# Kernel optimization log

Measured on AMD Instinct MI355X. Metric: run time of the kernel, lower is better.

## Reference

```python
import jax, jax.numpy as jnp
import numpy as np

# 5x5 Sobel kernels (exact constants from the torch module)
_GX5 = np.array([[2.,1.,1e-6,-1.,-2.],[3.,2.,1e-6,-2.,-3.],[4.,3.,0.,-3.,-4.],[3.,2.,1e-6,-2.,-3.],[2.,1.,1e-6,-1.,-2.]], np.float32)
_GY5 = np.array([[2.,3.,4.,3.,2.],[1.,2.,3.,2.,1.],[1e-6,1e-6,1e-6,1e-6,1e-6],[-1.,-2.,-3.,-2.,-1.],[-2.,-3.,-4.,-3.,-2.]], np.float32)


def _sobel(x):  # x: [B,1,H,W] -> [B,2,H,W] (gx, gy)
    k = jnp.stack([jnp.asarray(_GX5), jnp.asarray(_GY5)])[:, None]  # [2,1,5,5]
    return jax.lax.conv_general_dilated(x, k, (1, 1), 'SAME',
                                        dimension_numbers=('NCHW', 'OIHW', 'NCHW'))


def _quantize(gx, gy):
    # OrientQuantize: magnitude + orientation quantized to 8 bins
    div = 3.1416 / 8.0
    mag = jnp.sqrt(gx * gx + gy * gy + 1e-8)
    o = jnp.arctan2(gy, gx)
    conds = [
        (o >= div) & (o < 3 * div),
        (o >= 3 * div) & (o < 5 * div),
        (o >= 5 * div) & (o < 7 * div),
        ((o >= 7 * div) & (o < 8 * div)) | ((o >= -8 * div) & (o < -7 * div)),
        (o >= -7 * div) & (o < -5 * div),
        (o >= -5 * div) & (o < -3 * div),
        (o >= -3 * div) & (o < -div),
        (o >= -div) & (o < div),
    ]
    q = jnp.select(conds, [jnp.full_like(o, float(i)) for i in range(8)], 3.0)
    return mag, q.astype(jnp.int32)


def setup_inputs() -> dict:
    key = jax.random.key(0)
    k1, k2, k3 = jax.random.split(key, 3)
    return {
        'seg_map': jax.random.normal(k1, (2, 21, 256, 256), jnp.float32),
        'dense_ft': jax.random.normal(k2, (2, 256, 256, 256), jnp.float32),
        'mask': jax.random.normal(k3, (2, 21, 256, 256), jnp.float32),
        'label_with_bg': jnp.ones((2, 21), jnp.float32),
    }


def reference(seg_map, dense_ft, mask, label_with_bg):
    BETA, K, STEP = 1000.0, 100, 5
    n, C, h, w = seg_map.shape
    nfg, ch, hw = C - 1, dense_ft.shape[1], h * w

    # ---- Mix_fg: per-class Sobel orientation edges on sharpened softmax ----
    seg = jax.nn.softmax(seg_map * BETA, axis=1)[:, 1:]            # [n,nfg,h,w]
    edges = _sobel(seg.reshape(n * nfg, 1, h, w)).reshape(n, nfg, 2, h, w)
    label_fg = label_with_bg[:, 1:]                                 # [n,nfg]
    edges = edges * label_fg[:, :, None, None, None]
    mag, q = _quantize(edges[:, :, 0], edges[:, :, 1])              # [n,nfg,h,w]

    # ---- boundary pixels: strongest-K edge magnitudes per (b,c) ----
    _, pos = jax.lax.top_k(mag.reshape(n, nfg, hw), K)              # [n,nfg,K]
    o = jnp.take_along_axis(q.reshape(n, nfg, hw), pos, -1) + 1     # 1..8

    # ---- in_out_div: walk STEP pixels along/against gradient orientation ----
    mod4 = ((o % 4) == 0).astype(jnp.int32)
    horiz = ((o == 2) | (o == 6)).astype(jnp.int32)
    p_out = jnp.where(o < 4, STEP * STEP, -STEP)   # (-STEP)**(1+(o<4))
    p_in = jnp.where(o < 4, -STEP, 1)              # (-STEP)**(o<4)
    s_out = jnp.where(o % 2 == 0, -1, 1)           # (-1)**(1+o)
    s_in = -s_out                                   # (-1)**o
    out_idx = pos + p_out * mod4 * w + s_out * horiz
    in_idx = pos + p_in * mod4 * w + s_in * horiz

    def valid(x):
        return (x % (w - 1) != 0) & (x % (w - 1) != 1) & (x > 0) & (x < hw - 1)

    v_out, v_in = valid(out_idx), valid(in_idx)                     # [n,nfg,K] bool
    oi = jnp.clip(out_idx, 0, hw - 1)
    ii = jnp.clip(in_idx, 0, hw - 1)

    # ---- gather features / mask probs at walked positions ----
    dense = jax.nn.softmax(dense_ft, axis=1).reshape(n, ch, hw)
    msk = jax.nn.softmax(mask, axis=1).reshape(n, C, hw)
    b = jnp.arange(n)[:, None, None]
    outs = dense[b, :, oi]                                          # [n,nfg,K,ch]
    ins = jax.lax.stop_gradient(dense[b, :, ii])                    # detached
    outs_m = jax.lax.stop_gradient(msk[b, :, oi])
    ins_m = jax.lax.stop_gradient(msk[b, :, ii])

    sim = jnp.einsum('bcie,bcje->bcij', outs, ins)                  # [n,nfg,K,K]
    sim_m = jnp.einsum('bcie,bcje->bcij', outs_m, ins_m)

    fvi = v_in.astype(sim.dtype)
    fvo = v_out.astype(sim.dtype)
    ci = jnp.maximum(fvi.sum(-1), 1.0)
    co = jnp.maximum(fvo.sum(-1), 1.0)

    def rowmean(s):  # mean over in-samples -> [n,nfg,K]
        return (s * fvi[:, :, None, :]).sum(-1) / ci[..., None]

    def colmean(s):  # mean over out-samples -> [n,nfg,K]
        return (s * fvo[:, :, :, None]).sum(-2) / co[..., None]

    def gmean(s):    # global masked mean -> [n,nfg]
        num = (s * fvo[:, :, :, None] * fvi[:, :, None, :]).sum((-2, -1))
        return num / jnp.maximum(fvo.sum(-1) * fvi.sum(-1), 1.0)

    def beacon(sgn_mask, sgn_dense, vals, v):
        # loss_constructor: signed masked means over FP/FN/TP/TN categories
        def term(cat, sign):
            m = (cat & v).astype(vals.dtype)
            cnt = m.sum(-1)
            return sign * jnp.where(cnt > 0, (vals * m).sum(-1) / jnp.maximum(cnt, 1.0), 0.0)
        FP = sgn_mask & ~sgn_dense
        FN = ~sgn_mask & sgn_dense
        TP = ~sgn_mask & ~sgn_dense
        TN = sgn_mask & sgn_dense
        return term(FP, -1.0) + term(FN, 1.0) + term(TP, 1.0) + term(TN, -1.0)

    g = gmean(sim)
    gm = gmean(sim_m)
    rm, rmm = rowmean(sim), rowmean(sim_m)
    cm, cmm = colmean(sim), colmean(sim_m)
    sgn_rm = jax.lax.stop_gradient(rm) > g[..., None]
    sgn_rmm = rmm > gm[..., None]
    sgn_cm = jax.lax.stop_gradient(cm) > g[..., None]
    sgn_cmm = cmm > gm[..., None]

    loss_bc = beacon(sgn_rmm, sgn_rm, rm, v_out) + beacon(sgn_cmm, sgn_cm, cm, v_in)
    gate = ((v_in.sum(-1) >= 10) & (v_out.sum(-1) >= 10)).astype(loss_bc.dtype)
    gate = gate * (label_fg > 0).astype(loss_bc.dtype)
    return (loss_bc * gate).sum()
```

## Files before the change

kernel.cpp:

```cpp
#include <hip/hip_runtime.h>
#include <math.h>

#define HW 65536
#define WID 256
#define HEI 256
#define NB 2
#define NFG 20
#define NMAP 40
#define CH 256
#define CSEG 21
#define TK 100
#define PARTS 32
#define PARTN (HW / PARTS)
#define RPP (HEI / PARTS)
#define CAND (PARTS * TK)

__device__ __constant__ float c_GX[25] = {
  2.f,1.f,1e-6f,-1.f,-2.f,
  3.f,2.f,1e-6f,-2.f,-3.f,
  4.f,3.f,0.f,-3.f,-4.f,
  3.f,2.f,1e-6f,-2.f,-3.f,
  2.f,1.f,1e-6f,-1.f,-2.f};
__device__ __constant__ float c_GY[25] = {
  2.f,3.f,4.f,3.f,2.f,
  1.f,2.f,3.f,2.f,1.f,
  1e-6f,1e-6f,1e-6f,1e-6f,1e-6f,
  -1.f,-2.f,-3.f,-2.f,-1.f,
  -2.f,-3.f,-4.f,-3.f,-2.f};

__global__ __launch_bounds__(256) void k_seg(const float* __restrict__ seg_map,
                                             double* __restrict__ seg) {
  int idx = blockIdx.x * blockDim.x + threadIdx.x;
  if (idx >= NB * HW) return;
  int b = idx / HW, p = idx % HW;
  double x[CSEG];
  double m = -INFINITY;
  #pragma unroll
  for (int c = 0; c < CSEG; ++c) {
    double v = (double)seg_map[(size_t)(b * CSEG + c) * HW + p] * 1000.0;
    x[c] = v;
    m = fmax(m, v);
  }
  double s = 0.0;
  #pragma unroll
  for (int c = 0; c < CSEG; ++c) { double e = exp(x[c] - m); x[c] = e; s += e; }
  #pragma unroll
  for (int c = 1; c < CSEG; ++c)
    seg[(size_t)(b * NFG + (c - 1)) * HW + p] = x[c] / s;
}

__global__ __launch_bounds__(256) void k_sobel_topk(
    const double* __restrict__ seg, const float* __restrict__ label,
    unsigned char* __restrict__ qb,
    unsigned long long* __restrict__ ckey, int* __restrict__ cidx) {
  int mapi = blockIdx.x / PARTS, part = blockIdx.x % PARTS;
  int tid = threadIdx.x;
  int lane = tid & 63, w = tid >> 6;
  int row0 = part * RPP;
  const double* im = seg + (size_t)mapi * HW;

  __shared__ double tile[RPP + 4][WID];
  __shared__ unsigned int hist4[4][256];
  __shared__ int sfx[256];
  __shared__ int wtot[4];
  __shared__ int s_r, s_cnt, s_bsel;

  for (int r = 0; r < RPP + 4; ++r) {
    int gr = row0 - 2 + r;
    tile[r][tid] = (gr >= 0 && gr < HEI) ? im[gr * WID + tid] : 0.0;
  }
  if (tid == 0) { s_r = TK; s_cnt = 0; }
  __syncthreads();

  int b = mapi / NFG, c = mapi % NFG;
  double lab = (double)label[b * CSEG + c + 1];
  const double DIVQ = 3.1416 / 8.0;
  const double T1 = DIVQ, T3 = 3.0*DIVQ, T5 = 5.0*DIVQ, T7 = 7.0*DIVQ, T8 = 8.0*DIVQ;

  unsigned long long mykey[RPP];
  #pragma unroll
  for (int k = 0; k < RPP; ++k) {
    double gx = 0.0, gy = 0.0;
    #pragma unroll
    for (int dy = 0; dy < 5; ++dy) {
      #pragma unroll
      for (int dx = 0; dx < 5; ++dx) {
        int xx = tid + dx - 2;
        double v = (xx >= 0 && xx < WID) ? tile[k + dy][xx] : 0.0;
        gx += v * (double)c_GX[dy * 5 + dx];
        gy += v * (double)c_GY[dy * 5 + dx];
      }
    }
    gx *= lab; gy *= lab;
    double mg = sqrt(gx * gx + gy * gy + 1e-8);
    double o = atan2(gy, gx);
    int qv;
    if (o >= T1 && o < T3) qv = 0;
    else if (o >= T3 && o < T5) qv = 1;
    else if (o >= T5 && o < T7) qv = 2;
    else if ((o >= T7 && o < T8) || (o >= -T8 && o < -T7)) qv = 3;
    else if (o >= -T7 && o < -T5) qv = 4;
    else if (o >= -T5 && o < -T3) qv = 5;
    else if (o >= -T3 && o < -T1) qv = 6;
    else if (o >= -T1 && o < T1) qv = 7;
    else qv = 3;
    mykey[k] = (unsigned long long)__double_as_longlong(mg);
    qb[(size_t)mapi * HW + (size_t)(row0 + k) * WID + tid] = (unsigned char)qv;
  }
  __syncthreads();
  unsigned long long* sk = (unsigned long long*)&tile[0][0];
  #pragma unroll
  for (int k = 0; k < RPP; ++k) sk[k * WID + tid] = mykey[k];
  __syncthreads();

  unsigned long long pfx = 0ull, msk = 0ull;
  for (int round = 0; round < 8; ++round) {
    int shift = 56 - 8 * round;
    hist4[0][tid] = 0; hist4[1][tid] = 0; hist4[2][tid] = 0; hist4[3][tid] = 0;
    __syncthreads();
    #pragma unroll
    for (int k = 0; k < RPP; ++k) {
      unsigned long long key = sk[k * WID + tid];
      if ((key & msk) == pfx)
        atomicAdd(&hist4[w][(unsigned int)(key >> shift) & 0xFFu], 1u);
    }
    __syncthreads();
    int r = s_r;
    int v = (int)(hist4[0][tid] + hist4[1][tid] + hist4[2][tid] + hist4[3][tid]);
    #pragma unroll
    for (int off = 1; off < 64; off <<= 1) {
      int u = __shfl_down(v, off, 64);
      if (lane + off < 64) v += u;
    }
    if (lane == 0) wtot[w] = v;
    __syncthreads();
    int add = 0;
    for (int ww = w + 1; ww < 4; ++ww) add += wtot[ww];
    v += add;
    sfx[tid] = v;
    __syncthreads();
    int above = (tid == 255) ? 0 : sfx[tid + 1];
    if (v >= r && above < r) { s_bsel = tid; s_r = r - above; }
    __syncthreads();
    pfx |= ((unsigned long long)s_bsel << shift);
    msk |= (0xFFull << shift);
  }
  unsigned long long kv = pfx;
  int need_eq = s_r;

  unsigned long long* outk = ckey + (size_t)mapi * CAND + (size_t)part * TK;
  int* outi = cidx + (size_t)mapi * CAND + (size_t)part * TK;
  int gbase = part * PARTN;
  const int CHN = PARTN / 256;
  int base = tid * CHN;
  int myeq = 0;
  for (int k = 0; k < CHN; ++k) {
    unsigned long long key = sk[base + k];
    if (key > kv) {
      int slot = atomicAdd(&s_cnt, 1);
      outk[slot] = key; outi[slot] = gbase + base + k;
    } else if (key == kv) ++myeq;
  }
  int v2 = myeq;
  #pragma unroll
  for (int off = 1; off < 64; off <<= 1) {
    int u = __shfl_up(v2, off, 64);
    if (lane >= off) v2 += u;
  }
  if (lane == 63) wtot[w] = v2;
  __syncthreads();
  int addl = 0;
  for (int ww = 0; ww < w; ++ww) addl += wtot[ww];
  int incl = v2 + addl;
  int rank = incl - myeq;
  int eqtot = wtot[0] + wtot[1] + wtot[2] + wtot[3];
  int lo = eqtot - need_eq;
  int wb = TK - need_eq;
  for (int k = 0; k < CHN; ++k) {
    unsigned long long key = sk[base + k];
    if (key == kv) {
      if (rank >= lo) { outk[wb + rank - lo] = key; outi[wb + rank - lo] = gbase + base + k; }
      ++rank;
    }
  }
}

__global__ __launch_bounds__(256) void k_topk_merge(
    const unsigned long long* __restrict__ ckey,
    const int* __restrict__ cidx, int* __restrict__ pos) {
  int mapi = blockIdx.x, tid = threadIdx.x;
  int lane = tid & 63, w = tid >> 6;
  __shared__ unsigned long long k_[CAND];
  __shared__ int i_[CAND];
  __shared__ int eqi[CAND];
  __shared__ unsigned int hist4[4][256];
  __shared__ int sfx[256];
  __shared__ int wtot[4];
  __shared__ int s_r, s_cnt, s_eqn, s_bsel;
  for (int c = tid; c < CAND; c += 256) {
    k_[c] = ckey[(size_t)mapi * CAND + c];
    i_[c] = cidx[(size_t)mapi * CAND + c];
  }
  if (tid == 0) { s_r = TK; s_cnt = 0; s_eqn = 0; }
  __syncthreads();
  unsigned long long pfx = 0ull, msk = 0ull;
  for (int round = 0; round < 8; ++round) {
    int shift = 56 - 8 * round;
    hist4[0][tid] = 0; hist4[1][tid] = 0; hist4[2][tid] = 0; hist4[3][tid] = 0;
    __syncthreads();
    for (int c = tid; c < CAND; c += 256) {
      unsigned long long key = k_[c];
      if ((key & msk) == pfx)
        atomicAdd(&hist4[w][(unsigned int)(key >> shift) & 0xFFu], 1u);
    }
    __syncthreads();
    int r = s_r;
    int v = (int)(hist4[0][tid] + hist4[1][tid] + hist4[2][tid] + hist4[3][tid]);
    #pragma unroll
    for (int off = 1; off < 64; off <<= 1) {
      int u = __shfl_down(v, off, 64);
      if (lane + off < 64) v += u;
    }
    if (lane == 0) wtot[w] = v;
    __syncthreads();
    int add = 0;
    for (int ww = w + 1; ww < 4; ++ww) add += wtot[ww];
    v += add;
    sfx[tid] = v;
    __syncthreads();
    int above = (tid == 255) ? 0 : sfx[tid + 1];
    if (v >= r && above < r) { s_bsel = tid; s_r = r - above; }
    __syncthreads();
    pfx |= ((unsigned long long)s_bsel << shift);
    msk |= (0xFFull << shift);
  }
  unsigned long long kv = pfx;
  int need_eq = s_r;
  for (int c = tid; c < CAND; c += 256) {
    unsigned long long key = k_[c];
    if (key > kv) {
      int slot = atomicAdd(&s_cnt, 1);
      pos[mapi * TK + slot] = i_[c];
    } else if (key == kv) {
      int e = atomicAdd(&s_eqn, 1);
      eqi[e] = i_[c];
    }
  }
  __syncthreads();
  int eqn = s_eqn;
  int wb = TK - need_eq;
  for (int e = tid; e < eqn; e += 256) {
    int myi = eqi[e];
    int bigger = 0;
    for (int f = 0; f < eqn; ++f) bigger += (eqi[f] > myi) ? 1 : 0;
    if (bigger < need_eq) pos[mapi * TK + wb + bigger] = myi;
  }
}

__global__ __launch_bounds__(256) void k_gather(
    const float* __restrict__ dense_ft, const float* __restrict__ maskp,
    const unsigned char* __restrict__ qb, const int* __restrict__ pos,
    double* __restrict__ outs, double* __restrict__ ins,
    double* __restrict__ outs_m, double* __restrict__ ins_m,
    int* __restrict__ voutArr, int* __restrict__ vinArr) {
  int blk = blockIdx.x;
  int mapi = blk / TK, j = blk % TK;
  int b = mapi / NFG;
  int tid = threadIdx.x;
  int p = pos[mapi * TK + j];
  int o = (int)qb[(size_t)mapi * HW + p] + 1;
  int mod4 = ((o & 3) == 0) ? 1 : 0;
  int horiz = (o == 2 || o == 6) ? 1 : 0;
  int po = (o < 4) ? 25 : -5;
  int pi = (o < 4) ? -5 : 1;
  int so = ((o & 1) == 0) ? -1 : 1;
  int si = -so;
  int out_idx = p + po * mod4 * WID + so * horiz;
  int in_idx  = p + pi * mod4 * WID + si * horiz;
  int ro = out_idx % 255; if (ro < 0) ro += 255;
  int ri = in_idx  % 255; if (ri < 0) ri += 255;
  int vo = (ro != 0 && ro != 1 && out_idx > 0 && out_idx < HW - 1) ? 1 : 0;
  int vi = (ri != 0 && ri != 1 && in_idx  > 0 && in_idx  < HW - 1) ? 1 : 0;
  int oi = out_idx < 0 ? 0 : (out_idx > HW - 1 ? HW - 1 : out_idx);
  int ii = in_idx  < 0 ? 0 : (in_idx  > HW - 1 ? HW - 1 : in_idx);
  if (tid == 0) { voutArr[mapi * TK + j] = vo; vinArr[mapi * TK + j] = vi; }

  __shared__ double red[256];
  {
    double x = (double)dense_ft[(size_t)(b * CH + tid) * HW + oi];
    red[tid] = x; __syncthreads();
    for (int s = 128; s > 0; s >>= 1) { if (tid < s) red[tid] = fmax(red[tid], red[tid + s]); __syncthreads(); }
    double mx = red[0]; __syncthreads();
    double e = exp(x - mx);
    red[tid] = e; __syncthreads();
    for (int s = 128; s > 0; s >>= 1) { if (tid < s) red[tid] += red[tid + s]; __syncthreads(); }
    double sm = red[0]; __syncthreads();
    outs[((size_t)mapi * TK + j) * CH + tid] = e / sm;
  }
  {
    double x = (double)dense_ft[(size_t)(b * CH + tid) * HW + ii];
    red[tid] = x; __syncthreads();
    for (int s = 128; s > 0; s >>= 1) { if (tid < s) red[tid] = fmax(red[tid], red[tid + s]); __syncthreads(); }
    double mx = red[0]; __syncthreads();
    double e = exp(x - mx);
    red[tid] = e; __syncthreads();
    for (int s = 128; s > 0; s >>= 1) { if (tid < s) red[tid] += red[tid + s]; __syncthreads(); }
    double sm = red[0]; __syncthreads();
    ins[((size_t)mapi * TK + j) * CH + tid] = e / sm;
  }
  {
    double y = (tid < CSEG) ? (double)maskp[(size_t)(b * CSEG + tid) * HW + oi] : -INFINITY;
    red[tid] = y; __syncthreads();
    for (int s = 128; s > 0; s >>= 1) { if (tid < s) red[tid] = fmax(red[tid], red[tid + s]); __syncthreads(); }
    double mx = red[0]; __syncthreads();
    double e = (tid < CSEG) ? exp(y - mx) : 0.0;
    red[tid] = e; __syncthreads();
    for (int s = 128; s > 0; s >>= 1) { if (tid < s) red[tid] += red[tid + s]; __syncthreads(); }
    double sm = red[0]; __syncthreads();
    if (tid < CSEG) outs_m[((size_t)mapi * TK + j) * CSEG + tid] = e / sm;
    __syncthreads();
  }
  {
    double y = (tid < CSEG) ? (double)maskp[(size_t)(b * CSEG + tid) * HW + ii] : -INFINITY;
    red[tid] = y; __syncthreads();
    for (int s = 128; s > 0; s >>= 1) { if (tid < s) red[tid] = fmax(red[tid], red[tid + s]); __syncthreads(); }
    double mx = red[0]; __syncthreads();
    double e = (tid < CSEG) ? exp(y - mx) : 0.0;
    red[tid] = e; __syncthreads();
    for (int s = 128; s > 0; s >>= 1) { if (tid < s) red[tid] += red[tid + s]; __syncthreads(); }
    double sm = red[0]; __syncthreads();
    if (tid < CSEG) ins_m[((size_t)mapi * TK + j) * CSEG + tid] = e / sm;
  }
}

__global__ __launch_bounds__(256) void k_stats(
    const double* __restrict__ outs, const double* __restrict__ ins,
    const double* __restrict__ outs_m, const double* __restrict__ ins_m,
    const int* __restrict__ voutArr, const int* __restrict__ vinArr,
    const float* __restrict__ label, double* __restrict__ lossmap) {
  int mapi = blockIdx.x, tid = threadIdx.x;
  int b = mapi / NFG, c = mapi % NFG;
  __shared__ double fvo[TK], fvi[TK];
  __shared__ double avi[CH], avo[CH], avim[CSEG], avom[CSEG];
  __shared__ double rm[TK], cm[TK], rmm[TK], cmm[TK];
  __shared__ double s_sfvo, s_sfvi;
  if (tid < TK) {
    fvo[tid] = (double)voutArr[mapi * TK + tid];
    fvi[tid] = (double)vinArr[mapi * TK + tid];
  }
  __syncthreads();
  if (tid == 0) {
    double a = 0.0, d = 0.0;
    for (int j2 = 0; j2 < TK; ++j2) { a += fvo[j2]; d += fvi[j2]; }
    s_sfvo = a; s_sfvi = d;
  }
  const double* OUT  = outs   + (size_t)mapi * TK * CH;
  const double* IN   = ins    + (size_t)mapi * TK * CH;
  const double* OUTm = outs_m + (size_t)mapi * TK * CSEG;
  const double* INm  = ins_m  + (size_t)mapi * TK * CSEG;
  {
    double a = 0.0, d = 0.0;
    for (int j2 = 0; j2 < TK; ++j2) {
      a += IN[j2 * CH + tid] * fvi[j2];
      d += OUT[j2 * CH + tid] * fvo[j2];
    }
    avi[tid] = a; avo[tid] = d;
  }
  if (tid < CSEG) {
    double a = 0.0, d = 0.0;
    for (int j2 = 0; j2 < TK; ++j2) {
      a += INm[j2 * CSEG + tid] * fvi[j2];
      d += OUTm[j2 * CSEG + tid] * fvo[j2];
    }
    avim[tid] = a; avom[tid] = d;
  }
  __syncthreads();
  double ci = fmax(s_sfvi, 1.0), co = fmax(s_sfvo, 1.0);
  if (tid < TK) {
    double d1 = 0.0, d2 = 0.0, d3 = 0.0, d4 = 0.0;
    for (int e = 0; e < CH; ++e) { d1 += OUT[tid * CH + e] * avi[e]; d2 += IN[tid * CH + e] * avo[e]; }
    for (int e = 0; e < CSEG; ++e) { d3 += OUTm[tid * CSEG + e] * avim[e]; d4 += INm[tid * CSEG + e] * avom[e]; }
    rm[tid] = d1 / ci; cm[tid] = d2 / co; rmm[tid] = d3 / ci; cmm[tid] = d4 / co;
  }
  __syncthreads();
  if (tid == 0) {
    double g = 0.0, gm = 0.0;
    for (int e = 0; e < CH; ++e) g += avo[e] * avi[e];
    for (int e = 0; e < CSEG; ++e) gm += avom[e] * avim[e];
    double den = fmax(s_sfvo * s_sfvi, 1.0);
    g /= den; gm /= den;
    double loss = 0.0;
    {
      double s[4] = {0, 0, 0, 0}, cn[4] = {0, 0, 0, 0};
      for (int j2 = 0; j2 < TK; ++j2) {
        int smv = rmm[j2] > gm;
        int dmv = rm[j2] > g;
        int cat = smv ? (dmv ? 3 : 0) : (dmv ? 1 : 2);
        s[cat] += rm[j2] * fvo[j2];
        cn[cat] += fvo[j2];
      }
      const double sg[4] = {-1.0, 1.0, 1.0, -1.0};
      for (int t = 0; t < 4; ++t)
        if (cn[t] > 0.0) loss += sg[t] * (s[t] / fmax(cn[t], 1.0));
    }
    {
      double s[4] = {0, 0, 0, 0}, cn[4] = {0, 0, 0, 0};
      for (int j2 = 0; j2 < TK; ++j2) {
        int smv = cmm[j2] > gm;
        int dmv = cm[j2] > g;
        int cat = smv ? (dmv ? 3 : 0) : (dmv ? 1 : 2);
        s[cat] += cm[j2] * fvi[j2];
        cn[cat] += fvi[j2];
      }
      const double sg[4] = {-1.0, 1.0, 1.0, -1.0};
      for (int t = 0; t < 4; ++t)
        if (cn[t] > 0.0) loss += sg[t] * (s[t] / fmax(cn[t], 1.0));
    }
    float lab = label[b * CSEG + c + 1];
    double gate = (s_sfvi >= 10.0 && s_sfvo >= 10.0 && lab > 0.f) ? 1.0 : 0.0;
    lossmap[mapi] = loss * gate;
  }
}

__global__ __launch_bounds__(64) void k_final(const double* __restrict__ lossmap,
                                              float* __restrict__ out) {
  if (threadIdx.x == 0 && blockIdx.x == 0) {
    double s = 0.0;
    for (int i = 0; i < NMAP; ++i) s += lossmap[i];
    out[0] = (float)s;
  }
}

extern "C" void kernel_launch(void* const* d_in, const int* in_sizes, int n_in,
                              void* d_out, int out_size, void* d_ws, size_t ws_size,
                              hipStream_t stream) {
  const float* seg_map  = (const float*)d_in[0];
  const float* dense_ft = (const float*)d_in[1];
  const float* maskp    = (const float*)d_in[2];
  const float* label    = (const float*)d_in[3];
  float* outp = (float*)d_out;

  char* w = (char*)d_ws;
  double* seg = (double*)w;               w += (size_t)NB * NFG * HW * 8;
  double* outs   = (double*)w;            w += (size_t)NMAP * TK * CH * 8;
  double* ins    = (double*)w;            w += (size_t)NMAP * TK * CH * 8;
  double* outs_m = (double*)w;            w += (size_t)NMAP * TK * CSEG * 8;
  double* ins_m  = (double*)w;            w += (size_t)NMAP * TK * CSEG * 8;
  double* lossmap = (double*)w;           w += (size_t)NMAP * 8;
  unsigned long long* ckey = (unsigned long long*)w; w += (size_t)NMAP * CAND * 8;
  int* cidx = (int*)w;                    w += (size_t)NMAP * CAND * 4;
  int* pos  = (int*)w;                    w += (size_t)NMAP * TK * 4;
  int* vout = (int*)w;                    w += (size_t)NMAP * TK * 4;
  int* vin  = (int*)w;                    w += (size_t)NMAP * TK * 4;
  unsigned char* qb = (unsigned char*)w;  w += (size_t)NMAP * HW;

  k_seg<<<(NB * HW + 255) / 256, 256, 0, stream>>>(seg_map, seg);
  k_sobel_topk<<<NMAP * PARTS, 256, 0, stream>>>(seg, label, qb, ckey, cidx);
  k_topk_merge<<<NMAP, 256, 0, stream>>>(ckey, cidx, pos);
  k_gather<<<NMAP * TK, 256, 0, stream>>>(dense_ft, maskp, qb, pos, outs, ins,
                                          outs_m, ins_m, vout, vin);
  k_stats<<<NMAP, 256, 0, stream>>>(outs, ins, outs_m, ins_m, vout, vin, label, lossmap);
  k_final<<<1, 64, 0, stream>>>(lossmap, outp);
}
```

Baseline: 215.6 us.

## Replace barrier-heavy softmax reductions with per-wavefront shuffles and trim radix-select syncs

The gather/softmax kernel previously ran four block-wide tree reductions, each with many __syncthreads. It now gives each of the four wavefronts one softmax and reduces with 64-lane xor shuffles, with no block barriers. The radix-select loops in both top-k kernels zero the histogram once up front and clear it after reading, which drops one barrier and the shared suffix array per round. The per-pixel top-k also reads keys from registers instead of LDS, and the segmentation softmax skips exp for strongly underflowing inputs. Each wavefront now loads 4 strided dense_ft values per lane.

```diff
diff --git a/kernel.cpp b/kernel.cpp
--- a/kernel.cpp
+++ b/kernel.cpp
@@ -43,7 +43,11 @@
   }
   double s = 0.0;
   #pragma unroll
-  for (int c = 0; c < CSEG; ++c) { double e = exp(x[c] - m); x[c] = e; s += e; }
+  for (int c = 0; c < CSEG; ++c) {
+    double d = x[c] - m;
+    double e = (d < -746.0) ? 0.0 : exp(d);
+    x[c] = e; s += e;
+  }
   #pragma unroll
   for (int c = 1; c < CSEG; ++c)
     seg[(size_t)(b * NFG + (c - 1)) * HW + p] = x[c] / s;
@@ -61,7 +65,6 @@
 
   __shared__ double tile[RPP + 4][WID];
   __shared__ unsigned int hist4[4][256];
-  __shared__ int sfx[256];
   __shared__ int wtot[4];
   __shared__ int s_r, s_cnt, s_bsel;
 
@@ -69,6 +72,7 @@
     int gr = row0 - 2 + r;
     tile[r][tid] = (gr >= 0 && gr < HEI) ? im[gr * WID + tid] : 0.0;
   }
+  hist4[0][tid] = 0; hist4[1][tid] = 0; hist4[2][tid] = 0; hist4[3][tid] = 0;
   if (tid == 0) { s_r = TK; s_cnt = 0; }
   __syncthreads();
 
@@ -116,17 +120,17 @@
   unsigned long long pfx = 0ull, msk = 0ull;
   for (int round = 0; round < 8; ++round) {
     int shift = 56 - 8 * round;
-    hist4[0][tid] = 0; hist4[1][tid] = 0; hist4[2][tid] = 0; hist4[3][tid] = 0;
-    __syncthreads();
     #pragma unroll
     for (int k = 0; k < RPP; ++k) {
-      unsigned long long key = sk[k * WID + tid];
+      unsigned long long key = mykey[k];
       if ((key & msk) == pfx)
         atomicAdd(&hist4[w][(unsigned int)(key >> shift) & 0xFFu], 1u);
     }
     __syncthreads();
     int r = s_r;
-    int v = (int)(hist4[0][tid] + hist4[1][tid] + hist4[2][tid] + hist4[3][tid]);
+    int cnt = (int)(hist4[0][tid] + hist4[1][tid] + hist4[2][tid] + hist4[3][tid]);
+    hist4[0][tid] = 0; hist4[1][tid] = 0; hist4[2][tid] = 0; hist4[3][tid] = 0;
+    int v = cnt;
     #pragma unroll
     for (int off = 1; off < 64; off <<= 1) {
       int u = __shfl_down(v, off, 64);
@@ -137,10 +141,7 @@
     int add = 0;
     for (int ww = w + 1; ww < 4; ++ww) add += wtot[ww];
     v += add;
-    sfx[tid] = v;
-    __syncthreads();
-    int above = (tid == 255) ? 0 : sfx[tid + 1];
-    if (v >= r && above < r) { s_bsel = tid; s_r = r - above; }
+    if (v >= r && v - cnt < r) { s_bsel = tid; s_r = r - (v - cnt); }
     __syncthreads();
     pfx |= ((unsigned long long)s_bsel << shift);
     msk |= (0xFFull << shift);
@@ -194,20 +195,18 @@
   __shared__ int i_[CAND];
   __shared__ int eqi[CAND];
   __shared__ unsigned int hist4[4][256];
-  __shared__ int sfx[256];
   __shared__ int wtot[4];
   __shared__ int s_r, s_cnt, s_eqn, s_bsel;
   for (int c = tid; c < CAND; c += 256) {
     k_[c] = ckey[(size_t)mapi * CAND + c];
     i_[c] = cidx[(size_t)mapi * CAND + c];
   }
+  hist4[0][tid] = 0; hist4[1][tid] = 0; hist4[2][tid] = 0; hist4[3][tid] = 0;
   if (tid == 0) { s_r = TK; s_cnt = 0; s_eqn = 0; }
   __syncthreads();
   unsigned long long pfx = 0ull, msk = 0ull;
   for (int round = 0; round < 8; ++round) {
     int shift = 56 - 8 * round;
-    hist4[0][tid] = 0; hist4[1][tid] = 0; hist4[2][tid] = 0; hist4[3][tid] = 0;
-    __syncthreads();
     for (int c = tid; c < CAND; c += 256) {
       unsigned long long key = k_[c];
       if ((key & msk) == pfx)
@@ -215,7 +214,9 @@
     }
     __syncthreads();
     int r = s_r;
-    int v = (int)(hist4[0][tid] + hist4[1][tid] + hist4[2][tid] + hist4[3][tid]);
+    int cnt = (int)(hist4[0][tid] + hist4[1][tid] + hist4[2][tid] + hist4[3][tid]);
+    hist4[0][tid] = 0; hist4[1][tid] = 0; hist4[2][tid] = 0; hist4[3][tid] = 0;
+    int v = cnt;
     #pragma unroll
     for (int off = 1; off < 64; off <<= 1) {
       int u = __shfl_down(v, off, 64);
@@ -226,10 +227,7 @@
     int add = 0;
     for (int ww = w + 1; ww < 4; ++ww) add += wtot[ww];
     v += add;
-    sfx[tid] = v;
-    __syncthreads();
-    int above = (tid == 255) ? 0 : sfx[tid + 1];
-    if (v >= r && above < r) { s_bsel = tid; s_r = r - above; }
+    if (v >= r && v - cnt < r) { s_bsel = tid; s_r = r - (v - cnt); }
     __syncthreads();
     pfx |= ((unsigned long long)s_bsel << shift);
     msk |= (0xFFull << shift);
@@ -267,6 +265,7 @@
   int mapi = blk / TK, j = blk % TK;
   int b = mapi / NFG;
   int tid = threadIdx.x;
+  int lane = tid & 63, w = tid >> 6;
   int p = pos[mapi * TK + j];
   int o = (int)qb[(size_t)mapi * HW + p] + 1;
   int mod4 = ((o & 3) == 0) ? 1 : 0;
@@ -285,51 +284,38 @@
   int ii = in_idx  < 0 ? 0 : (in_idx  > HW - 1 ? HW - 1 : in_idx);
   if (tid == 0) { voutArr[mapi * TK + j] = vo; vinArr[mapi * TK + j] = vi; }
 
-  __shared__ double red[256];
-  {
-    double x = (double)dense_ft[(size_t)(b * CH + tid) * HW + oi];
-    red[tid] = x; __syncthreads();
-    for (int s = 128; s > 0; s >>= 1) { if (tid < s) red[tid] = fmax(red[tid], red[tid + s]); __syncthreads(); }
-    double mx = red[0]; __syncthreads();
-    double e = exp(x - mx);
-    red[tid] = e; __syncthreads();
-    for (int s = 128; s > 0; s >>= 1) { if (tid < s) red[tid] += red[tid + s]; __syncthreads(); }
-    double sm = red[0]; __syncthreads();
-    outs[((size_t)mapi * TK + j) * CH + tid] = e / sm;
-  }
-  {
-    double x = (double)dense_ft[(size_t)(b * CH + tid) * HW + ii];
-    red[tid] = x; __syncthreads();
-    for (int s = 128; s > 0; s >>= 1) { if (tid < s) red[tid] = fmax(red[tid], red[tid + s]); __syncthreads(); }
-    double mx = red[0]; __syncthreads();
-    double e = exp(x - mx);
-    red[tid] = e; __syncthreads();
-    for (int s = 128; s > 0; s >>= 1) { if (tid < s) red[tid] += red[tid + s]; __syncthreads(); }
-    double sm = red[0]; __syncthreads();
-    ins[((size_t)mapi * TK + j) * CH + tid] = e / sm;
-  }
-  {
-    double y = (tid < CSEG) ? (double)maskp[(size_t)(b * CSEG + tid) * HW + oi] : -INFINITY;
-    red[tid] = y; __syncthreads();
-    for (int s = 128; s > 0; s >>= 1) { if (tid < s) red[tid] = fmax(red[tid], red[tid + s]); __syncthreads(); }
-    double mx = red[0]; __syncthreads();
-    double e = (tid < CSEG) ? exp(y - mx) : 0.0;
-    red[tid] = e; __syncthreads();
-    for (int s = 128; s > 0; s >>= 1) { if (tid < s) red[tid] += red[tid + s]; __syncthreads(); }
-    double sm = red[0]; __syncthreads();
-    if (tid < CSEG) outs_m[((size_t)mapi * TK + j) * CSEG + tid] = e / sm;
-    __syncthreads();
-  }
-  {
-    double y = (tid < CSEG) ? (double)maskp[(size_t)(b * CSEG + tid) * HW + ii] : -INFINITY;
-    red[tid] = y; __syncthreads();
-    for (int s = 128; s > 0; s >>= 1) { if (tid < s) red[tid] = fmax(red[tid], red[tid + s]); __syncthreads(); }
-    double mx = red[0]; __syncthreads();
-    double e = (tid < CSEG) ? exp(y - mx) : 0.0;
-    red[tid] = e; __syncthreads();
-    for (int s = 128; s > 0; s >>= 1) { if (tid < s) red[tid] += red[tid + s]; __syncthreads(); }
-    double sm = red[0]; __syncthreads();
-    if (tid < CSEG) ins_m[((size_t)mapi * TK + j) * CSEG + tid] = e / sm;
+  if (w < 2) {
+    int idx = (w == 0) ? oi : ii;
+    double x[4];
+    double mx = -INFINITY;
+    #pragma unroll
+    for (int q = 0; q < 4; ++q) {
+      x[q] = (double)dense_ft[(size_t)(b * CH + lane + 64 * q) * HW + idx];
+      mx = fmax(mx, x[q]);
+    }
+    #pragma unroll
+    for (int off = 1; off < 64; off <<= 1) mx = fmax(mx, __shfl_xor(mx, off, 64));
+    double e[4], s = 0.0;
+    #pragma unroll
+    for (int q = 0; q < 4; ++q) { e[q] = exp(x[q] - mx); s += e[q]; }
+    #pragma unroll
+    for (int off = 1; off < 64; off <<= 1) s += __shfl_xor(s, off, 64);
+    double* dst = ((w == 0) ? outs : ins) + ((size_t)mapi * TK + j) * CH;
+    #pragma unroll
+    for (int q = 0; q < 4; ++q) dst[lane + 64 * q] = e[q] / s;
+  } else {
+    int idx = (w == 2) ? oi : ii;
+    double y = (lane < CSEG) ? (double)maskp[(size_t)(b * CSEG + lane) * HW + idx]
+                             : -INFINITY;
+    double mx = y;
+    #pragma unroll
+    for (int off = 1; off < 64; off <<= 1) mx = fmax(mx, __shfl_xor(mx, off, 64));
+    double e = (lane < CSEG) ? exp(y - mx) : 0.0;
+    double s = e;
+    #pragma unroll
+    for (int off = 1; off < 64; off <<= 1) s += __shfl_xor(s, off, 64);
+    if (lane < CSEG)
+      (((w == 2) ? outs_m : ins_m) + ((size_t)mapi * TK + j) * CSEG)[lane] = e / s;
   }
 }
 
```

Result: faster. 199.5 us (-7.4%).
